# Performance work log

Hardware: AMD Instinct MI355X
Metric: run time of the kernel (lower is better)

Reference implementation:

```python
import jax, jax.numpy as jnp
import numpy as np

LRELU_SLOPE = 0.2
ACT_GAIN = float(np.sqrt(2.0))  # def_gain of lrelu in StyleGAN2
CLAMP = 256.0


def _affine(w, W, b):
    # StyleGAN2 FullyConnectedLayer: runtime weight gain 1/sqrt(in_features)
    return w @ W.T * (1.0 / np.sqrt(W.shape[1])) + b[None, :]


def _gather(x, fn, pad):
    # zero rows for padding faces appended at the end, then neighborhood gather
    padded = jnp.concatenate([x, jnp.zeros((pad, x.shape[1]), x.dtype)], axis=0)
    return padded[fn]  # [N, K, C]


def _mod_texture_conv(g, styles, wc, wsd, wcr):
    # g: [N, 9, I] gathered neighborhoods; styles: [B, I]
    B, I = styles.shape
    N = g.shape[0]
    F = N // B
    # position-typed 1x1 weights: [self, 4 sides, 4 corners] -> [O, I, 9]
    W = jnp.concatenate([wc[:, :, None],
                         jnp.repeat(wsd[:, :, None], 4, axis=2),
                         jnp.repeat(wcr[:, :, None], 4, axis=2)], axis=2)
    wmod = W[None] * styles[:, None, :, None]                    # [B,O,I,9] modulate
    d = jax.lax.rsqrt(jnp.sum(wmod * wmod, axis=(2, 3)) + 1e-8)  # [B,O] demodulate
    wmod = wmod * d[:, :, None, None]
    out = jnp.einsum('bfki,boik->bfok', g.reshape(B, F, 9, I), wmod)
    return out.max(axis=3).reshape(N, -1)  # MaxPool2d((1,9)) aggregation


def _smooth_upsample(x, pool_map, fn, pad):
    # replicate coarse face features to fine faces, then smooth over 9-neighborhood
    return _gather(x[pool_map], fn, pad).mean(axis=1)


def _act(x, bias):
    # clamp_gain(lrelu(x+b), act_gain*gain, 256*gain) with gain=1
    return jnp.clip(jax.nn.leaky_relu(x + bias[None, :], LRELU_SLOPE) * ACT_GAIN, -CLAMP, CLAMP)


def setup_inputs() -> dict:
    key = jax.random.key(0)
    ks = iter(jax.random.split(key, 40))
    B, Fc, Ff = 1, 32768, 131072
    IN, OUT, GEO, COL, WD = 128, 128, 32, 3, 512
    OC1 = OUT - GEO  # 96
    PAD0, PAD1 = 1024, 4096
    nk = lambda *s: jax.random.normal(next(ks), s, jnp.float32)
    ri = lambda shape, hi: jax.random.randint(next(ks), shape, 0, hi, jnp.int32).astype(jnp.int64)
    return dict(
        x=nk(B * Fc, IN - GEO), shape_feat=nk(B * Fc, GEO), img=nk(B * Fc, COL),
        ws=nk(B, 3, WD),
        fn0=ri((B * Fc, 9), B * Fc + PAD0), fn1=ri((B * Ff, 9), B * Ff + PAD1),
        pool_map0=ri((B * Ff,), B * Fc),
        pad0=PAD0, pad1=PAD1,
        affine0_w=nk(IN, WD), affine0_b=jnp.ones((IN,), jnp.float32),
        w_center0=nk(OUT, IN), w_side0=nk(OUT, IN), w_corner0=nk(OUT, IN),
        noise_strength0=nk(1) * 0.1, bias0=nk(OUT) * 0.1, noise_const0=nk(Ff),
        affine1_w=nk(OUT, WD), affine1_b=jnp.ones((OUT,), jnp.float32),
        w_center1=nk(OC1, OUT), w_side1=nk(OC1, OUT), w_corner1=nk(OC1, OUT),
        noise_strength1=nk(1) * 0.1, bias1=nk(OC1) * 0.1, noise_const1=nk(Ff),
        affine2_w=nk(OC1, WD), affine2_b=jnp.ones((OC1,), jnp.float32),
        w_rgb=nk(COL, OC1), bias_rgb=nk(COL) * 0.1,
    )


def reference(x, shape_feat, img, ws, fn0, fn1, pool_map0, pad0, pad1,
              affine0_w, affine0_b, w_center0, w_side0, w_corner0,
              noise_strength0, bias0, noise_const0,
              affine1_w, affine1_b, w_center1, w_side1, w_corner1,
              noise_strength1, bias1, noise_const1,
              affine2_w, affine2_b, w_rgb, bias_rgb):
    B = ws.shape[0]
    h = jnp.concatenate([x, shape_feat], axis=1)  # [B*Fc, IN]
    # ---- conv0: coarse-level modulated face conv, then SmoothUpsample to fine ----
    s0 = _affine(ws[:, 0], affine0_w, affine0_b)
    h = _mod_texture_conv(_gather(h, fn0, pad0), s0, w_center0, w_side0, w_corner0)
    h = _smooth_upsample(h, pool_map0, fn1, pad1)  # [B*Ff, OUT]
    h = h + jnp.tile(noise_const0[None, :], (B, 1)).reshape(-1, 1) * noise_strength0
    h = _act(h, bias0)
    # ---- conv1: fine-level modulated face conv ----
    s1 = _affine(ws[:, 1], affine1_w, affine1_b)
    h = _mod_texture_conv(_gather(h, fn1, pad1), s1, w_center1, w_side1, w_corner1)
    h = h + jnp.tile(noise_const1[None, :], (B, 1)).reshape(-1, 1) * noise_strength1
    h = _act(h, bias1)  # [B*Ff, 96]
    # ---- torgb: 1x1 modulated conv (demodulate=False), weight_gain on styles ----
    s2 = _affine(ws[:, 2], affine2_w, affine2_b) * (1.0 / np.sqrt(w_rgb.shape[1]))
    xg = _gather(h, fn1[:, :1], pad1)[:, 0]  # kernel_size^2 == 1 -> self gather
    y = jnp.einsum('bfi,oi,bi->bfo', xg.reshape(B, -1, xg.shape[1]), w_rgb, s2)
    y = jnp.clip(y.reshape(xg.shape[0], -1) + bias_rgb[None, :], -CLAMP, CLAMP)
    img_out = _smooth_upsample(img, pool_map0, fn1, pad1) + y
    return h, img_out
```

## Files before the change

### kernel.cpp

```cpp
#include <hip/hip_runtime.h>

#define FC 32768
#define FF 131072
#define LRELU_SLOPE 0.2f
#define ACT_GAIN 1.4142135623730951f
#define CLAMP_V 256.0f

typedef __bf16 bf16x8 __attribute__((ext_vector_type(8)));
typedef float f32x4 __attribute__((ext_vector_type(4)));
typedef float f32x2 __attribute__((ext_vector_type(2)));
typedef unsigned u32x4 __attribute__((ext_vector_type(4)));
typedef unsigned u32x2 __attribute__((ext_vector_type(2)));
typedef unsigned short u16x4 __attribute__((ext_vector_type(4)));

static __device__ __forceinline__ unsigned short f2bf(float f) {
    unsigned u = __float_as_uint(f);
    u += 0x7FFFu + ((u >> 16) & 1u);
    return (unsigned short)(u >> 16);
}
static __device__ __forceinline__ unsigned packbf(float a, float b) {
    return (unsigned)f2bf(a) | ((unsigned)f2bf(b) << 16);
}
static __device__ __forceinline__ float bf2f(unsigned short u) {
    return __uint_as_float(((unsigned)u) << 16);
}
static __device__ __forceinline__ float actf(float v) {
    v = (v < 0.f) ? v * LRELU_SLOPE : v;
    v *= ACT_GAIN;
    return fminf(fmaxf(v, -CLAMP_V), CLAMP_V);
}

__global__ void k_prep2(const float* __restrict__ wsvec,
                        const float* __restrict__ a0w, const float* __restrict__ a0b,
                        const float* __restrict__ a1w, const float* __restrict__ a1b,
                        const float* __restrict__ a2w, const float* __restrict__ a2b,
                        float* __restrict__ s0, float* __restrict__ s1, float* __restrict__ s2,
                        unsigned* __restrict__ zrow)
{
    int lane = threadIdx.x & 63;
    int t = blockIdx.x * 4 + (threadIdx.x >> 6);
    if (t >= 352) {
        if (t == 352) zrow[lane] = 0u;
        return;
    }
    int level, o;
    const float *W, *bptr; float* out;
    if (t < 128)       { level = 0; o = t;       W = a0w; bptr = a0b; out = s0; }
    else if (t < 256)  { level = 1; o = t - 128; W = a1w; bptr = a1b; out = s1; }
    else               { level = 2; o = t - 256; W = a2w; bptr = a2b; out = s2; }
    const float* wrow = wsvec + level * 512;
    const float* Wr = W + (size_t)o * 512;
    f32x4 wa = *(const f32x4*)(wrow + lane * 8);
    f32x4 wb = *(const f32x4*)(wrow + lane * 8 + 4);
    f32x4 va = *(const f32x4*)(Wr + lane * 8);
    f32x4 vb = *(const f32x4*)(Wr + lane * 8 + 4);
    float acc = wa.x * va.x + wa.y * va.y + wa.z * va.z + wa.w * va.w
              + wb.x * vb.x + wb.y * vb.y + wb.z * vb.z + wb.w * vb.w;
    #pragma unroll
    for (int off = 32; off; off >>= 1) acc += __shfl_down(acc, off, 64);
    if (lane == 0) {
        float v = acc * 0.04419417382415922f + bptr[o];
        if (level == 2) v *= 0.10206207261596577f;
        out[o] = v;
    }
}

__global__ void k_misc(const float* __restrict__ x, const float* __restrict__ sf,
                       u16x4* __restrict__ xcat,
                       const int* __restrict__ fn1, const int* __restrict__ pmap,
                       int* __restrict__ cidx)
{
    int b = blockIdx.x;
    if (b < FC * 32 / 256) {
        int gid = b * 256 + threadIdx.x;
        int f = gid >> 5;
        int c4 = (gid & 31) * 4;
        f32x4 v;
        if (c4 < 96) v = *(const f32x4*)(x + (size_t)f * 96 + c4);
        else         v = *(const f32x4*)(sf + (size_t)f * 32 + (c4 - 96));
        u16x4 o;
        o.x = f2bf(v.x); o.y = f2bf(v.y); o.z = f2bf(v.z); o.w = f2bf(v.w);
        xcat[gid] = o;
    } else {
        int gid = (b - FC * 32 / 256) * 256 + threadIdx.x;
        int g = fn1[gid];
        cidx[gid] = ((unsigned)g < FF) ? pmap[g] : -1;
    }
}

__global__ void k_wmod(const float* __restrict__ wc0, const float* __restrict__ wsd0,
                       const float* __restrict__ wcr0, const float* __restrict__ s0,
                       unsigned short* __restrict__ wm0,
                       const float* __restrict__ wc1, const float* __restrict__ wsd1,
                       const float* __restrict__ wcr1, const float* __restrict__ s1,
                       unsigned short* __restrict__ wm1,
                       const float* __restrict__ wrgb, const float* __restrict__ s2,
                       float* __restrict__ wrgbmod)
{
    int b = blockIdx.x;
    int i = threadIdx.x;
    if (b == 224) {
        for (int t = i; t < 288; t += 128) {
            int c = t / 96, k = t % 96;
            wrgbmod[c * 96 + k] = wrgb[c * 96 + k] * s2[k];
        }
        return;
    }
    const float *wc, *wsd, *wcr, *s; unsigned short* out; int o, O;
    if (b < 128) { wc = wc0; wsd = wsd0; wcr = wcr0; s = s0; out = wm0; o = b; O = 128; }
    else         { wc = wc1; wsd = wsd1; wcr = wcr1; s = s1; out = wm1; o = b - 128; O = 96; }
    float sv = s[i];
    float pc = wc[o * 128 + i] * sv;
    float ps = wsd[o * 128 + i] * sv;
    float pr = wcr[o * 128 + i] * sv;
    float part = pc * pc + 4.f * ps * ps + 4.f * pr * pr;
    __shared__ float red[2];
    #pragma unroll
    for (int off = 32; off; off >>= 1) part += __shfl_down(part, off, 64);
    if ((threadIdx.x & 63) == 0) red[threadIdx.x >> 6] = part;
    __syncthreads();
    float d = rsqrtf(red[0] + red[1] + 1e-8f);
    out[(0 * O + o) * 128 + i] = f2bf(pc * d);
    out[(1 * O + o) * 128 + i] = f2bf(ps * d);
    out[(2 * O + o) * 128 + i] = f2bf(pr * d);
}

__launch_bounds__(256, 2)
__global__ void k_fgemm0(const unsigned short* __restrict__ xcat,
                         const unsigned short* __restrict__ wm,
                         const int* __restrict__ fn0,
                         const unsigned* __restrict__ zrow,
                         unsigned* __restrict__ hc0)
{
    __shared__ char ldsw[65536];
    int lane = threadIdx.x & 63;
    int w = threadIdx.x >> 6;
    int fbase = (blockIdx.x * 4 + w) * 16;
    int quad = lane >> 4, l15 = lane & 15;
    int face = fbase + l15;
    const char* hb = (const char*)xcat;
    const char* wb = (const char*)wm;

    #pragma unroll
    for (int i0 = 0; i0 < 16; ++i0) {
        int i = i0 * 256 + threadIdx.x;
        u32x4 v = *(const u32x4*)(wb + 32768 + (size_t)i * 16);
        int r = i >> 4, c = i & 15;
        *(u32x4*)(ldsw + r * 256 + ((c ^ (r & 7)) * 16)) = v;
    }
    __syncthreads();

    int id[9];
    #pragma unroll
    for (int j = 0; j < 9; ++j) id[j] = fn0[(size_t)face * 9 + j];

    f32x4 ymax[8];
    #pragma unroll
    for (int mt = 0; mt < 8; ++mt)
        #pragma unroll
        for (int r = 0; r < 4; ++r) ymax[mt][r] = -3.0e38f;

    int xr = l15 & 7;

    #pragma unroll
    for (int j = 0; j < 9; ++j) {
        const int t = (j == 0) ? 0 : ((j < 5) ? 1 : 2);
        const char* src = ((unsigned)id[j] < FC) ? (hb + (size_t)id[j] * 256) : (const char*)zrow;
        bf16x8 bfr[4];
        #pragma unroll
        for (int s = 0; s < 4; ++s)
            bfr[s] = *(const bf16x8*)(src + s * 64 + quad * 16);
        f32x4 acc[8];
        #pragma unroll
        for (int mt = 0; mt < 8; ++mt)
            #pragma unroll
            for (int r = 0; r < 4; ++r) acc[mt][r] = 0.f;
        #pragma unroll
        for (int s = 0; s < 4; ++s) {
            #pragma unroll
            for (int mt = 0; mt < 8; ++mt) {
                bf16x8 afr;
                if (t == 0)
                    afr = *(const bf16x8*)(wb + (size_t)(((mt * 16 + l15) * 128 + s * 32 + quad * 8) * 2));
                else
                    afr = *(const bf16x8*)(ldsw + ((t - 1) * 128 + mt * 16 + l15) * 256
                                                + (((s * 4 + quad) ^ xr) * 16));
                acc[mt] = __builtin_amdgcn_mfma_f32_16x16x32_bf16(afr, bfr[s], acc[mt], 0, 0, 0);
            }
        }
        #pragma unroll
        for (int mt = 0; mt < 8; ++mt)
            #pragma unroll
            for (int r = 0; r < 4; ++r)
                ymax[mt][r] = fmaxf(ymax[mt][r], acc[mt][r]);
    }

    #pragma unroll
    for (int mt = 0; mt < 8; ++mt) {
        u32x2 v;
        v.x = packbf(ymax[mt][0], ymax[mt][1]);
        v.y = packbf(ymax[mt][2], ymax[mt][3]);
        *(u32x2*)(hc0 + (size_t)face * 64 + mt * 8 + quad * 2) = v;
    }
}

__global__ void k_upsample(const unsigned* __restrict__ hc, const int* __restrict__ cidx,
                           const float* __restrict__ nco0,
                           const float* __restrict__ ns0p, const float* __restrict__ bias0,
                           unsigned* __restrict__ h1u, const unsigned* __restrict__ zrow)
{
    int gid = blockIdx.x * 256 + threadIdx.x;
    int f = gid >> 4;
    int c = gid & 15;
    int id[9];
    #pragma unroll
    for (int j = 0; j < 9; ++j) id[j] = cidx[f * 9 + j];
    u32x4 v[9];
    #pragma unroll
    for (int j = 0; j < 9; ++j) {
        const unsigned* p = (id[j] >= 0) ? (hc + (size_t)id[j] * 64) : zrow;
        v[j] = *(const u32x4*)(p + c * 4);
    }
    float nz = nco0[f] * ns0p[0];
    f32x4 b0 = *(const f32x4*)(bias0 + c * 8);
    f32x4 b1 = *(const f32x4*)(bias0 + c * 8 + 4);
    const float inv9 = 1.f / 9.f;
    u32x4 out;
    #pragma unroll
    for (int k = 0; k < 4; ++k) {
        float a0 = 0.f, a1 = 0.f;
        #pragma unroll
        for (int j = 0; j < 9; ++j) {
            a0 += bf2f((unsigned short)v[j][k]);
            a1 += bf2f((unsigned short)(v[j][k] >> 16));
        }
        float bb0 = (k < 2) ? ((k == 0) ? b0.x : b0.z) : ((k == 2) ? b1.x : b1.z);
        float bb1 = (k < 2) ? ((k == 0) ? b0.y : b0.w) : ((k == 2) ? b1.y : b1.w);
        a0 = actf(a0 * inv9 + nz + bb0);
        a1 = actf(a1 * inv9 + nz + bb1);
        out[k] = packbf(a0, a1);
    }
    *(u32x4*)(h1u + (size_t)f * 64 + c * 4) = out;
}

__launch_bounds__(256, 2)
__global__ void k_fgemm1(const unsigned short* __restrict__ h1,
                         const unsigned short* __restrict__ wm,
                         const int* __restrict__ fn1,
                         const unsigned* __restrict__ zrow,
                         const float* __restrict__ nco1, const float* __restrict__ ns1p,
                         const float* __restrict__ bias1, const float* __restrict__ wrgbmod,
                         float* __restrict__ hout, f32x4* __restrict__ rgb3)
{
    __shared__ char ldsw[49152];
    int lane = threadIdx.x & 63;
    int w = threadIdx.x >> 6;
    int fbase = (blockIdx.x * 4 + w) * 16;
    int quad = lane >> 4, l15 = lane & 15;
    int face = fbase + l15;
    const char* hb = (const char*)h1;
    const char* wb = (const char*)wm;

    #pragma unroll
    for (int i0 = 0; i0 < 12; ++i0) {
        int i = i0 * 256 + threadIdx.x;
        u32x4 v = *(const u32x4*)(wb + 24576 + (size_t)i * 16);
        int r = i >> 4, c = i & 15;
        *(u32x4*)(ldsw + r * 256 + ((c ^ (r & 7)) * 16)) = v;
    }
    __syncthreads();

    int id[9];
    #pragma unroll
    for (int j = 0; j < 9; ++j) id[j] = fn1[(size_t)face * 9 + j];

    f32x4 ymax[6];
    #pragma unroll
    for (int mt = 0; mt < 6; ++mt)
        #pragma unroll
        for (int r = 0; r < 4; ++r) ymax[mt][r] = -3.0e38f;

    int xr = l15 & 7;

    #pragma unroll
    for (int j = 0; j < 9; ++j) {
        const int t = (j == 0) ? 0 : ((j < 5) ? 1 : 2);
        const char* src = ((unsigned)id[j] < FF) ? (hb + (size_t)id[j] * 256) : (const char*)zrow;
        bf16x8 bfr[4];
        #pragma unroll
        for (int s = 0; s < 4; ++s)
            bfr[s] = *(const bf16x8*)(src + s * 64 + quad * 16);
        f32x4 acc[6];
        #pragma unroll
        for (int mt = 0; mt < 6; ++mt)
            #pragma unroll
            for (int r = 0; r < 4; ++r) acc[mt][r] = 0.f;
        #pragma unroll
        for (int s = 0; s < 4; ++s) {
            #pragma unroll
            for (int mt = 0; mt < 6; ++mt) {
                bf16x8 afr;
                if (t == 0)
                    afr = *(const bf16x8*)(wb + (size_t)(((mt * 16 + l15) * 128 + s * 32 + quad * 8) * 2));
                else
                    afr = *(const bf16x8*)(ldsw + ((t - 1) * 96 + mt * 16 + l15) * 256
                                                + (((s * 4 + quad) ^ xr) * 16));
                acc[mt] = __builtin_amdgcn_mfma_f32_16x16x32_bf16(afr, bfr[s], acc[mt], 0, 0, 0);
            }
        }
        #pragma unroll
        for (int mt = 0; mt < 6; ++mt)
            #pragma unroll
            for (int r = 0; r < 4; ++r)
                ymax[mt][r] = fmaxf(ymax[mt][r], acc[mt][r]);
    }

    float ns1 = ns1p[0];
    float nz = nco1[face] * ns1;
    float p0 = 0.f, p1 = 0.f, p2 = 0.f;
    #pragma unroll
    for (int mt = 0; mt < 6; ++mt) {
        f32x4 bv = *(const f32x4*)(bias1 + mt * 16 + quad * 4);
        f32x4 hv;
        #pragma unroll
        for (int r = 0; r < 4; ++r) hv[r] = actf(ymax[mt][r] + nz + bv[r]);
        __builtin_nontemporal_store(hv, (f32x4*)(hout + (size_t)face * 96 + mt * 16 + quad * 4));
        f32x4 w0 = *(const f32x4*)(wrgbmod + mt * 16 + quad * 4);
        f32x4 w1 = *(const f32x4*)(wrgbmod + 96 + mt * 16 + quad * 4);
        f32x4 w2 = *(const f32x4*)(wrgbmod + 192 + mt * 16 + quad * 4);
        p0 += hv.x * w0.x + hv.y * w0.y + hv.z * w0.z + hv.w * w0.w;
        p1 += hv.x * w1.x + hv.y * w1.y + hv.z * w1.z + hv.w * w1.w;
        p2 += hv.x * w2.x + hv.y * w2.y + hv.z * w2.z + hv.w * w2.w;
    }
    p0 += __shfl_xor(p0, 16, 64); p0 += __shfl_xor(p0, 32, 64);
    p1 += __shfl_xor(p1, 16, 64); p1 += __shfl_xor(p1, 32, 64);
    p2 += __shfl_xor(p2, 16, 64); p2 += __shfl_xor(p2, 32, 64);
    if (quad == 0) {
        f32x4 o; o.x = p0; o.y = p1; o.z = p2; o.w = 0.f;
        rgb3[face] = o;
    }
}

__global__ void k_torgb2(const f32x4* __restrict__ rgb3, const int* __restrict__ fn1,
                         const int* __restrict__ cidx, const float* __restrict__ img,
                         const float* __restrict__ brgb, float* __restrict__ imgout)
{
    int f = blockIdx.x * 256 + threadIdx.x;
    int g0 = fn1[(size_t)f * 9];
    float y0 = 0.f, y1 = 0.f, y2 = 0.f;
    if ((unsigned)g0 < FF) {
        f32x4 y = rgb3[g0];
        y0 = y.x; y1 = y.y; y2 = y.z;
    }
    y0 = fminf(fmaxf(y0 + brgb[0], -CLAMP_V), CLAMP_V);
    y1 = fminf(fmaxf(y1 + brgb[1], -CLAMP_V), CLAMP_V);
    y2 = fminf(fmaxf(y2 + brgb[2], -CLAMP_V), CLAMP_V);
    float i0 = 0.f, i1 = 0.f, i2 = 0.f;
    #pragma unroll
    for (int j = 0; j < 9; ++j) {
        int id = cidx[f * 9 + j];
        if (id >= 0) {
            const float* ir = img + (size_t)id * 3;
            i0 += ir[0]; i1 += ir[1]; i2 += ir[2];
        }
    }
    const float inv9 = 1.f / 9.f;
    imgout[(size_t)f * 3 + 0] = i0 * inv9 + y0;
    imgout[(size_t)f * 3 + 1] = i1 * inv9 + y1;
    imgout[(size_t)f * 3 + 2] = i2 * inv9 + y2;
}

extern "C" void kernel_launch(void* const* d_in, const int* in_sizes, int n_in,
                              void* d_out, int out_size, void* d_ws, size_t ws_size,
                              hipStream_t stream) {
    const float* x     = (const float*)d_in[0];
    const float* sfeat = (const float*)d_in[1];
    const float* img   = (const float*)d_in[2];
    const float* wsv   = (const float*)d_in[3];
    const int* fn0     = (const int*)d_in[4];
    const int* fn1     = (const int*)d_in[5];
    const int* pmap    = (const int*)d_in[6];
    const float* a0w   = (const float*)d_in[9];
    const float* a0b   = (const float*)d_in[10];
    const float* wc0   = (const float*)d_in[11];
    const float* wsd0  = (const float*)d_in[12];
    const float* wcr0  = (const float*)d_in[13];
    const float* ns0   = (const float*)d_in[14];
    const float* bias0 = (const float*)d_in[15];
    const float* nco0  = (const float*)d_in[16];
    const float* a1w   = (const float*)d_in[17];
    const float* a1b   = (const float*)d_in[18];
    const float* wc1   = (const float*)d_in[19];
    const float* wsd1  = (const float*)d_in[20];
    const float* wcr1  = (const float*)d_in[21];
    const float* ns1   = (const float*)d_in[22];
    const float* bias1 = (const float*)d_in[23];
    const float* nco1  = (const float*)d_in[24];
    const float* a2w   = (const float*)d_in[25];
    const float* a2b   = (const float*)d_in[26];
    const float* wrgb  = (const float*)d_in[27];
    const float* brgb  = (const float*)d_in[28];

    char* wsb = (char*)d_ws;
    float* s0            = (float*)(wsb + 0);
    float* s1            = (float*)(wsb + 512);
    float* s2            = (float*)(wsb + 1024);
    float* wrgbmod       = (float*)(wsb + 1536);
    unsigned* zrow       = (unsigned*)(wsb + 4096);
    unsigned short* wm0  = (unsigned short*)(wsb + 8192);
    unsigned short* wm1  = (unsigned short*)(wsb + 8192 + 98304);
    unsigned short* xcat = (unsigned short*)(wsb + 262144);
    unsigned* hc0        = (unsigned*)(wsb + 33816576);
    unsigned short* h1   = (unsigned short*)(wsb + 42205184);
    int* cidx            = (int*)(wsb + 75759616);
    f32x4* rgb3          = (f32x4*)(wsb + 155975680);

    float* out_h   = (float*)d_out;
    float* out_img = out_h + (size_t)FF * 96;

    k_misc<<<FC * 32 / 256 + FF * 9 / 256, 256, 0, stream>>>(x, sfeat, (u16x4*)xcat, fn1, pmap, cidx);
    k_prep2<<<89, 256, 0, stream>>>(wsv, a0w, a0b, a1w, a1b, a2w, a2b, s0, s1, s2, zrow);
    k_wmod<<<225, 128, 0, stream>>>(wc0, wsd0, wcr0, s0, wm0,
                                    wc1, wsd1, wcr1, s1, wm1, wrgb, s2, wrgbmod);
    k_fgemm0<<<FC / 64, 256, 0, stream>>>(xcat, wm0, fn0, zrow, hc0);
    k_upsample<<<FF * 16 / 256, 256, 0, stream>>>(hc0, cidx, nco0, ns0, bias0, (unsigned*)h1, zrow);
    k_fgemm1<<<FF / 64, 256, 0, stream>>>(h1, wm1, fn1, zrow, nco1, ns1, bias1, wrgbmod,
                                          out_h, rgb3);
    k_torgb2<<<FF / 256, 256, 0, stream>>>(rgb3, fn1, cidx, img, brgb, out_img);
}
```

Measured before the change: 314.0 us.

## Split neighbor positions across wave pairs in face GEMMs and add XCD block swizzle

Each 16-face group in the two face-conv GEMM kernels is now handled by two waves instead of one. One wave takes the self and side neighbors and the other takes the corner neighbors, and the partial maxima are combined through LDS after a barrier. Grids double so each block covers 32 faces, which gives more parallel work per face and a shorter dependent MFMA chain per wave. Block indices are also remapped so neighboring blocks land on the same XCD, aiming for better L2 locality. In exchange, the weight tiles are loaded into LDS twice as often in total, and each block adds two barriers plus an LDS round trip.

```diff
diff --git a/kernel.cpp b/kernel.cpp
--- a/kernel.cpp
+++ b/kernel.cpp
@@ -28,6 +28,9 @@
     v = (v < 0.f) ? v * LRELU_SLOPE : v;
     v *= ACT_GAIN;
     return fminf(fmaxf(v, -CLAMP_V), CLAMP_V);
+}
+static __device__ __forceinline__ int xcd_swz(int bid, int nwg) {
+    return (bid & 7) * (nwg >> 3) + (bid >> 3);
 }
 
 __global__ void k_prep2(const float* __restrict__ wsvec,
@@ -125,6 +128,41 @@
     out[(2 * O + o) * 128 + i] = f2bf(pr * d);
 }
 
+template<int TT>
+static __device__ __forceinline__ void step0(int idv, const char* hb, const char* wb,
+                                             const char* ldsw, const unsigned* zrow,
+                                             int quad, int l15, int xr, f32x4 (&ymax)[8])
+{
+    const char* src = ((unsigned)idv < FC) ? (hb + (size_t)idv * 256) : (const char*)zrow;
+    bf16x8 bfr[4];
+    #pragma unroll
+    for (int s = 0; s < 4; ++s)
+        bfr[s] = *(const bf16x8*)(src + s * 64 + quad * 16);
+    f32x4 acc[8];
+    #pragma unroll
+    for (int mt = 0; mt < 8; ++mt)
+        #pragma unroll
+        for (int r = 0; r < 4; ++r) acc[mt][r] = 0.f;
+    #pragma unroll
+    for (int s = 0; s < 4; ++s) {
+        #pragma unroll
+        for (int mt = 0; mt < 8; ++mt) {
+            bf16x8 afr;
+            if (TT == 0)
+                afr = *(const bf16x8*)(wb + (size_t)(((mt * 16 + l15) * 128 + s * 32 + quad * 8) * 2));
+            else
+                afr = *(const bf16x8*)(ldsw + ((TT - 1) * 128 + mt * 16 + l15) * 256
+                                            + (((s * 4 + quad) ^ xr) * 16));
+            acc[mt] = __builtin_amdgcn_mfma_f32_16x16x32_bf16(afr, bfr[s], acc[mt], 0, 0, 0);
+        }
+    }
+    #pragma unroll
+    for (int mt = 0; mt < 8; ++mt)
+        #pragma unroll
+        for (int r = 0; r < 4; ++r)
+            ymax[mt][r] = fmaxf(ymax[mt][r], acc[mt][r]);
+}
+
 __launch_bounds__(256, 2)
 __global__ void k_fgemm0(const unsigned short* __restrict__ xcat,
                          const unsigned short* __restrict__ wm,
@@ -133,9 +171,12 @@
                          unsigned* __restrict__ hc0)
 {
     __shared__ char ldsw[65536];
+    int bid = xcd_swz(blockIdx.x, gridDim.x);
     int lane = threadIdx.x & 63;
     int w = threadIdx.x >> 6;
-    int fbase = (blockIdx.x * 4 + w) * 16;
+    int fgrp = w >> 1;
+    int wq = w & 1;
+    int fbase = (bid * 2 + fgrp) * 16;
     int quad = lane >> 4, l15 = lane & 15;
     int face = fbase + l15;
     const char* hb = (const char*)xcat;
@@ -150,9 +191,12 @@
     }
     __syncthreads();
 
-    int id[9];
-    #pragma unroll
-    for (int j = 0; j < 9; ++j) id[j] = fn0[(size_t)face * 9 + j];
+    int id[5];
+    #pragma unroll
+    for (int k = 0; k < 5; ++k) {
+        int jj = wq ? (4 + k) : ((k < 4) ? k : 4);
+        id[k] = fn0[(size_t)face * 9 + jj];
+    }
 
     f32x4 ymax[8];
     #pragma unroll
@@ -162,45 +206,38 @@
 
     int xr = l15 & 7;
 
-    #pragma unroll
-    for (int j = 0; j < 9; ++j) {
-        const int t = (j == 0) ? 0 : ((j < 5) ? 1 : 2);
-        const char* src = ((unsigned)id[j] < FC) ? (hb + (size_t)id[j] * 256) : (const char*)zrow;
-        bf16x8 bfr[4];
-        #pragma unroll
-        for (int s = 0; s < 4; ++s)
-            bfr[s] = *(const bf16x8*)(src + s * 64 + quad * 16);
-        f32x4 acc[8];
+    if (wq == 0) {
+        step0<0>(id[0], hb, wb, ldsw, zrow, quad, l15, xr, ymax);
+        step0<1>(id[1], hb, wb, ldsw, zrow, quad, l15, xr, ymax);
+        step0<1>(id[2], hb, wb, ldsw, zrow, quad, l15, xr, ymax);
+        step0<1>(id[3], hb, wb, ldsw, zrow, quad, l15, xr, ymax);
+    } else {
+        step0<1>(id[0], hb, wb, ldsw, zrow, quad, l15, xr, ymax);
+        step0<2>(id[1], hb, wb, ldsw, zrow, quad, l15, xr, ymax);
+        step0<2>(id[2], hb, wb, ldsw, zrow, quad, l15, xr, ymax);
+        step0<2>(id[3], hb, wb, ldsw, zrow, quad, l15, xr, ymax);
+        step0<2>(id[4], hb, wb, ldsw, zrow, quad, l15, xr, ymax);
+    }
+
+    __syncthreads();
+    float* cmb = (float*)ldsw;
+    if (wq == 1) {
         #pragma unroll
         for (int mt = 0; mt < 8; ++mt)
+            *(f32x4*)(cmb + (fgrp * 16 + l15) * 132 + mt * 16 + quad * 4) = ymax[mt];
+    }
+    __syncthreads();
+    if (wq == 0) {
+        #pragma unroll
+        for (int mt = 0; mt < 8; ++mt) {
+            f32x4 o = *(const f32x4*)(cmb + (fgrp * 16 + l15) * 132 + mt * 16 + quad * 4);
             #pragma unroll
-            for (int r = 0; r < 4; ++r) acc[mt][r] = 0.f;
-        #pragma unroll
-        for (int s = 0; s < 4; ++s) {
-            #pragma unroll
-            for (int mt = 0; mt < 8; ++mt) {
-                bf16x8 afr;
-                if (t == 0)
-                    afr = *(const bf16x8*)(wb + (size_t)(((mt * 16 + l15) * 128 + s * 32 + quad * 8) * 2));
-                else
-                    afr = *(const bf16x8*)(ldsw + ((t - 1) * 128 + mt * 16 + l15) * 256
-                                                + (((s * 4 + quad) ^ xr) * 16));
-                acc[mt] = __builtin_amdgcn_mfma_f32_16x16x32_bf16(afr, bfr[s], acc[mt], 0, 0, 0);
-            }
-        }
-        #pragma unroll
-        for (int mt = 0; mt < 8; ++mt)
-            #pragma unroll
-            for (int r = 0; r < 4; ++r)
-                ymax[mt][r] = fmaxf(ymax[mt][r], acc[mt][r]);
-    }
-
-    #pragma unroll
-    for (int mt = 0; mt < 8; ++mt) {
-        u32x2 v;
-        v.x = packbf(ymax[mt][0], ymax[mt][1]);
-        v.y = packbf(ymax[mt][2], ymax[mt][3]);
-        *(u32x2*)(hc0 + (size_t)face * 64 + mt * 8 + quad * 2) = v;
+            for (int r = 0; r < 4; ++r) ymax[mt][r] = fmaxf(ymax[mt][r], o[r]);
+            u32x2 v;
+            v.x = packbf(ymax[mt][0], ymax[mt][1]);
+            v.y = packbf(ymax[mt][2], ymax[mt][3]);
+            *(u32x2*)(hc0 + (size_t)face * 64 + mt * 8 + quad * 2) = v;
+        }
     }
 }
 
@@ -209,7 +246,8 @@
                            const float* __restrict__ ns0p, const float* __restrict__ bias0,
                            unsigned* __restrict__ h1u, const unsigned* __restrict__ zrow)
 {
-    int gid = blockIdx.x * 256 + threadIdx.x;
+    int bid = xcd_swz(blockIdx.x, gridDim.x);
+    int gid = bid * 256 + threadIdx.x;
     int f = gid >> 4;
     int c = gid & 15;
     int id[9];
@@ -241,6 +279,41 @@
         out[k] = packbf(a0, a1);
     }
     *(u32x4*)(h1u + (size_t)f * 64 + c * 4) = out;
+}
+
+template<int TT>
+static __device__ __forceinline__ void step1(int idv, const char* hb, const char* wb,
+                                             const char* ldsw, const unsigned* zrow,
+                                             int quad, int l15, int xr, f32x4 (&ymax)[6])
+{
+    const char* src = ((unsigned)idv < FF) ? (hb + (size_t)idv * 256) : (const char*)zrow;
+    bf16x8 bfr[4];
+    #pragma unroll
+    for (int s = 0; s < 4; ++s)
+        bfr[s] = *(const bf16x8*)(src + s * 64 + quad * 16);
+    f32x4 acc[6];
+    #pragma unroll
+    for (int mt = 0; mt < 6; ++mt)
+        #pragma unroll
+        for (int r = 0; r < 4; ++r) acc[mt][r] = 0.f;
+    #pragma unroll
+    for (int s = 0; s < 4; ++s) {
+        #pragma unroll
+        for (int mt = 0; mt < 6; ++mt) {
+            bf16x8 afr;
+            if (TT == 0)
+                afr = *(const bf16x8*)(wb + (size_t)(((mt * 16 + l15) * 128 + s * 32 + quad * 8) * 2));
+            else
+                afr = *(const bf16x8*)(ldsw + ((TT - 1) * 96 + mt * 16 + l15) * 256
+                                            + (((s * 4 + quad) ^ xr) * 16));
+            acc[mt] = __builtin_amdgcn_mfma_f32_16x16x32_bf16(afr, bfr[s], acc[mt], 0, 0, 0);
+        }
+    }
+    #pragma unroll
+    for (int mt = 0; mt < 6; ++mt)
+        #pragma unroll
+        for (int r = 0; r < 4; ++r)
+            ymax[mt][r] = fmaxf(ymax[mt][r], acc[mt][r]);
 }
 
 __launch_bounds__(256, 2)
@@ -253,9 +326,12 @@
                          float* __restrict__ hout, f32x4* __restrict__ rgb3)
 {
     __shared__ char ldsw[49152];
+    int bid = xcd_swz(blockIdx.x, gridDim.x);
     int lane = threadIdx.x & 63;
     int w = threadIdx.x >> 6;
-    int fbase = (blockIdx.x * 4 + w) * 16;
+    int fgrp = w >> 1;
+    int wq = w & 1;
+    int fbase = (bid * 2 + fgrp) * 16;
     int quad = lane >> 4, l15 = lane & 15;
     int face = fbase + l15;
     const char* hb = (const char*)h1;
@@ -270,9 +346,12 @@
     }
     __syncthreads();
 
-    int id[9];
-    #pragma unroll
-    for (int j = 0; j < 9; ++j) id[j] = fn1[(size_t)face * 9 + j];
+    int id[5];
+    #pragma unroll
+    for (int k = 0; k < 5; ++k) {
+        int jj = wq ? (4 + k) : ((k < 4) ? k : 4);
+        id[k] = fn1[(size_t)face * 9 + jj];
+    }
 
     f32x4 ymax[6];
     #pragma unroll
@@ -282,62 +361,54 @@
 
     int xr = l15 & 7;
 
-    #pragma unroll
-    for (int j = 0; j < 9; ++j) {
-        const int t = (j == 0) ? 0 : ((j < 5) ? 1 : 2);
-        const char* src = ((unsigned)id[j] < FF) ? (hb + (size_t)id[j] * 256) : (const char*)zrow;
-        bf16x8 bfr[4];
-        #pragma unroll
-        for (int s = 0; s < 4; ++s)
-            bfr[s] = *(const bf16x8*)(src + s * 64 + quad * 16);
-        f32x4 acc[6];
+    if (wq == 0) {
+        step1<0>(id[0], hb, wb, ldsw, zrow, quad, l15, xr, ymax);
+        step1<1>(id[1], hb, wb, ldsw, zrow, quad, l15, xr, ymax);
+        step1<1>(id[2], hb, wb, ldsw, zrow, quad, l15, xr, ymax);
+        step1<1>(id[3], hb, wb, ldsw, zrow, quad, l15, xr, ymax);
+    } else {
+        step1<1>(id[0], hb, wb, ldsw, zrow, quad, l15, xr, ymax);
+        step1<2>(id[1], hb, wb, ldsw, zrow, quad, l15, xr, ymax);
+        step1<2>(id[2], hb, wb, ldsw, zrow, quad, l15, xr, ymax);
+        step1<2>(id[3], hb, wb, ldsw, zrow, quad, l15, xr, ymax);
+        step1<2>(id[4], hb, wb, ldsw, zrow, quad, l15, xr, ymax);
+    }
+
+    __syncthreads();
+    float* cmb = (float*)ldsw;
+    if (wq == 1) {
         #pragma unroll
         for (int mt = 0; mt < 6; ++mt)
-            #pragma unroll
-            for (int r = 0; r < 4; ++r) acc[mt][r] = 0.f;
-        #pragma unroll
-        for (int s = 0; s < 4; ++s) {
-            #pragma unroll
-            for (int mt = 0; mt < 6; ++mt) {
-                bf16x8 afr;
-                if (t == 0)
-                    afr = *(const bf16x8*)(wb + (size_t)(((mt * 16 + l15) * 128 + s * 32 + quad * 8) * 2));
-                else
-                    afr = *(const bf16x8*)(ldsw + ((t - 1) * 96 + mt * 16 + l15) * 256
-                                                + (((s * 4 + quad) ^ xr) * 16));
-                acc[mt] = __builtin_amdgcn_mfma_f32_16x16x32_bf16(afr, bfr[s], acc[mt], 0, 0, 0);
-            }
-        }
-        #pragma unroll
-        for (int mt = 0; mt < 6; ++mt)
+            *(f32x4*)(cmb + (fgrp * 16 + l15) * 100 + mt * 16 + quad * 4) = ymax[mt];
+    }
+    __syncthreads();
+    if (wq == 0) {
+        float ns1 = ns1p[0];
+        float nz = nco1[face] * ns1;
+        float p0 = 0.f, p1 = 0.f, p2 = 0.f;
+        #pragma unroll
+        for (int mt = 0; mt < 6; ++mt) {
+            f32x4 o = *(const f32x4*)(cmb + (fgrp * 16 + l15) * 100 + mt * 16 + quad * 4);
+            f32x4 bv = *(const f32x4*)(bias1 + mt * 16 + quad * 4);
+            f32x4 hv;
             #pragma unroll
             for (int r = 0; r < 4; ++r)
-                ymax[mt][r] = fmaxf(ymax[mt][r], acc[mt][r]);
-    }
-
-    float ns1 = ns1p[0];
-    float nz = nco1[face] * ns1;
-    float p0 = 0.f, p1 = 0.f, p2 = 0.f;
-    #pragma unroll
-    for (int mt = 0; mt < 6; ++mt) {
-        f32x4 bv = *(const f32x4*)(bias1 + mt * 16 + quad * 4);
-        f32x4 hv;
-        #pragma unroll
-        for (int r = 0; r < 4; ++r) hv[r] = actf(ymax[mt][r] + nz + bv[r]);
-        __builtin_nontemporal_store(hv, (f32x4*)(hout + (size_t)face * 96 + mt * 16 + quad * 4));
-        f32x4 w0 = *(const f32x4*)(wrgbmod + mt * 16 + quad * 4);
-        f32x4 w1 = *(const f32x4*)(wrgbmod + 96 + mt * 16 + quad * 4);
-        f32x4 w2 = *(const f32x4*)(wrgbmod + 192 + mt * 16 + quad * 4);
-        p0 += hv.x * w0.x + hv.y * w0.y + hv.z * w0.z + hv.w * w0.w;
-        p1 += hv.x * w1.x + hv.y * w1.y + hv.z * w1.z + hv.w * w1.w;
-        p2 += hv.x * w2.x + hv.y * w2.y + hv.z * w2.z + hv.w * w2.w;
-    }
-    p0 += __shfl_xor(p0, 16, 64); p0 += __shfl_xor(p0, 32, 64);
-    p1 += __shfl_xor(p1, 16, 64); p1 += __shfl_xor(p1, 32, 64);
-    p2 += __shfl_xor(p2, 16, 64); p2 += __shfl_xor(p2, 32, 64);
-    if (quad == 0) {
-        f32x4 o; o.x = p0; o.y = p1; o.z = p2; o.w = 0.f;
-        rgb3[face] = o;
+                hv[r] = actf(fmaxf(ymax[mt][r], o[r]) + nz + bv[r]);
+            __builtin_nontemporal_store(hv, (f32x4*)(hout + (size_t)face * 96 + mt * 16 + quad * 4));
+            f32x4 w0 = *(const f32x4*)(wrgbmod + mt * 16 + quad * 4);
+            f32x4 w1 = *(const f32x4*)(wrgbmod + 96 + mt * 16 + quad * 4);
+            f32x4 w2 = *(const f32x4*)(wrgbmod + 192 + mt * 16 + quad * 4);
+            p0 += hv.x * w0.x + hv.y * w0.y + hv.z * w0.z + hv.w * w0.w;
+            p1 += hv.x * w1.x + hv.y * w1.y + hv.z * w1.z + hv.w * w1.w;
+            p2 += hv.x * w2.x + hv.y * w2.y + hv.z * w2.z + hv.w * w2.w;
+        }
+        p0 += __shfl_xor(p0, 16, 64); p0 += __shfl_xor(p0, 32, 64);
+        p1 += __shfl_xor(p1, 16, 64); p1 += __shfl_xor(p1, 32, 64);
+        p2 += __shfl_xor(p2, 16, 64); p2 += __shfl_xor(p2, 32, 64);
+        if (quad == 0) {
+            f32x4 o; o.x = p0; o.y = p1; o.z = p2; o.w = 0.f;
+            rgb3[face] = o;
+        }
     }
 }
 
@@ -422,9 +493,9 @@
     k_prep2<<<89, 256, 0, stream>>>(wsv, a0w, a0b, a1w, a1b, a2w, a2b, s0, s1, s2, zrow);
     k_wmod<<<225, 128, 0, stream>>>(wc0, wsd0, wcr0, s0, wm0,
                                     wc1, wsd1, wcr1, s1, wm1, wrgb, s2, wrgbmod);
-    k_fgemm0<<<FC / 64, 256, 0, stream>>>(xcat, wm0, fn0, zrow, hc0);
+    k_fgemm0<<<FC / 32, 256, 0, stream>>>(xcat, wm0, fn0, zrow, hc0);
     k_upsample<<<FF * 16 / 256, 256, 0, stream>>>(hc0, cidx, nco0, ns0, bias0, (unsigned*)h1, zrow);
-    k_fgemm1<<<FF / 64, 256, 0, stream>>>(h1, wm1, fn1, zrow, nco1, ns1, bias1, wrgbmod,
+    k_fgemm1<<<FF / 32, 256, 0, stream>>>(h1, wm1, fn1, zrow, nco1, ns1, bias1, wrgbmod,
                                           out_h, rgb3);
     k_torgb2<<<FF / 256, 256, 0, stream>>>(rgb3, fn1, cidx, img, brgb, out_img);
 }
```

Result: faster. 283.0 us (-9.9%).
